# Optimization experiments

Hardware: AMD Instinct MI355X
Metric: run time of the kernel (lower is better)

The kernel has to match this reference:

```python
import jax, jax.numpy as jnp
import numpy as np
import math

WINDOW_LEFT = 512   # sliding-window: each query attends to keys in [q-512, q]
WINDOW_RIGHT = 0    # causal
NEG_INF = -1e30


def setup_inputs() -> dict:
    key = jax.random.key(0)
    kq, kk, kv, ks = jax.random.split(key, 4)
    B, S, H, D = 2, 2048, 16, 128
    q = jax.random.normal(kq, (B, S, H, D), dtype=jnp.float32)
    k = jax.random.normal(kk, (B, S, H, D), dtype=jnp.float32)
    v = jax.random.normal(kv, (B, S, H, D), dtype=jnp.float32)
    # geometric-ish ALiBi slopes per head (positive, decaying), like flash-attn
    alibi_slopes = jax.random.uniform(ks, (H,), dtype=jnp.float32, minval=0.001, maxval=0.5)
    return {"q": q, "k": k, "v": v, "alibi_slopes": alibi_slopes}


def reference(q, k, v, alibi_slopes):
    # q,k,v: [B, S, H, D]; alibi_slopes: [H]
    B, S, H, D = q.shape
    scale = 1.0 / math.sqrt(D)
    # scores: [B, H, Sq, Sk]
    scores = jnp.einsum("bqhd,bkhd->bhqk", q, k) * scale
    qi = jnp.arange(S)[:, None]
    ki = jnp.arange(S)[None, :]
    rel = ki - qi  # [Sq, Sk], <=0 for past keys
    # ALiBi bias (equal q/k lengths): -slope * |q - k|
    alibi = -alibi_slopes[:, None, None] * jnp.abs(rel).astype(scores.dtype)  # [H,Sq,Sk]
    scores = scores + alibi[None, :, :, :]
    # causal + sliding-window mask: allow WINDOW_RIGHT future, WINDOW_LEFT past
    mask = (rel <= WINDOW_RIGHT) & (rel >= -WINDOW_LEFT)  # [Sq, Sk]
    scores = jnp.where(mask[None, None, :, :], scores, NEG_INF)
    p = jax.nn.softmax(scores, axis=-1)
    out = jnp.einsum("bhqk,bkhd->bqhd", p, v)
    return out
```

## Files before the change

### kernel.cpp

```cpp
#include <hip/hip_runtime.h>
#include <hip/hip_bf16.h>

typedef __attribute__((ext_vector_type(8))) __bf16 bf16x8;
typedef __attribute__((ext_vector_type(4))) __bf16 bf16x4;
typedef __attribute__((ext_vector_type(2))) __bf16 bf16x2;
typedef __attribute__((ext_vector_type(4))) float f32x4;

#define MFMA32(a, b, c) __builtin_amdgcn_mfma_f32_16x16x32_bf16((a), (b), (c), 0, 0, 0)

constexpr int Bc = 2, Sc = 2048, Hc = 16, Dc = 128;
constexpr int HD = Hc * Dc;
constexpr int QB = 128;
constexpr float SCALE = 0.0883883476483184405f;
constexpr float NEGF = -30000.0f;
constexpr int KSTR = 2080;

__device__ inline bf16x8 cvt8(f32x4 a, f32x4 b) {
    bf16x8 r;
    r[0]=(__bf16)a[0]; r[1]=(__bf16)a[1]; r[2]=(__bf16)a[2]; r[3]=(__bf16)a[3];
    r[4]=(__bf16)b[0]; r[5]=(__bf16)b[1]; r[6]=(__bf16)b[2]; r[7]=(__bf16)b[3];
    return r;
}

__global__ __launch_bounds__(256, 2) void lumen_attn_kernel(
    const float* __restrict__ Q, const float* __restrict__ K,
    const float* __restrict__ V, const float* __restrict__ SLP,
    float* __restrict__ O)
{
    __shared__ __align__(16) char k_lds[64 * 256];
    __shared__ __align__(16) char v_lds[8 * KSTR];
    __shared__ __align__(16) char p_lds[4][32 * 128];

    const int tid  = threadIdx.x;
    const int lane = tid & 63;
    const int wid  = tid >> 6;
    const int cl = lane & 15;
    const int kg = lane >> 4;
    const int r0 = kg << 2;

    const int bid = blockIdx.x;
    const int swz = (bid & 7) * 64 + (bid >> 3);
    const int qb  = (swz & 15) * QB;
    const int bh  = swz >> 4;
    const int h = bh & 15, b = bh >> 4;

    const float slope = SLP[h];
    const size_t base = (size_t)b * Sc * HD + (size_t)h * Dc;
    const float* qp = Q + base;
    const float* kp = K + base;
    const float* vp = V + base;
    float*       op = O + base;

    const int qw = qb + wid * 32;

    bf16x8 qf[2][4];
    #pragma unroll
    for (int s = 0; s < 2; ++s) {
        const float* qrow = qp + (size_t)(qw + s * 16 + cl) * HD + kg * 8;
        #pragma unroll
        for (int c = 0; c < 4; ++c) {
            f32x4 a = *(const f32x4*)(qrow + c * 32);
            f32x4 bq = *(const f32x4*)(qrow + c * 32 + 4);
            #pragma unroll
            for (int i = 0; i < 4; ++i) { a[i] *= SCALE; bq[i] *= SCALE; }
            qf[s][c] = cvt8(a, bq);
        }
    }

    f32x4 o_acc[2][8];
    #pragma unroll
    for (int s = 0; s < 2; ++s)
        #pragma unroll
        for (int nn = 0; nn < 8; ++nn) o_acc[s][nn] = f32x4{0.f, 0.f, 0.f, 0.f};
    float ssum[2] = {0.f, 0.f};

    int voff[8];
    #pragma unroll
    for (int nn = 0; nn < 8; ++nn) {
        const int d = nn * 16 + cl;
        const int s = (d & ~7) | ((d & 7) ^ ((d >> 3) & 7));
        voff[nn] = s * 16;
    }

    const int kb0    = qb > 512 ? qb - 512 : 0;
    const int kb_end = qb + QB - 64;

    const int tk5 = tid >> 3;
    const int t8  = tid & 7;
    const int d0  = t8 * 16;

    char* const pw = p_lds[wid];
    const int swp = (cl & 7) << 4;

    for (int kb = kb0; kb <= kb_end; kb += 64) {
        __syncthreads();

        #pragma unroll
        for (int p = 0; p < 2; ++p) {
            const int k = p * 32 + tk5;
            const float* kr = kp + (size_t)(kb + k) * HD + d0;
            bf16x8 kA = cvt8(*(const f32x4*)kr,       *(const f32x4*)(kr + 4));
            bf16x8 kB = cvt8(*(const f32x4*)(kr + 8), *(const f32x4*)(kr + 12));
            char* kbse = k_lds + k * 256;
            const int sw = (k & 15) << 4;
            *(bf16x8*)(kbse + ((d0 * 2) ^ sw))      = kA;
            *(bf16x8*)(kbse + ((d0 * 2 + 16) ^ sw)) = kB;
        }
        {
            const float* v0_ = vp + (size_t)(kb + 2 * tk5) * HD + d0;
            const float* v1_ = v0_ + HD;
            bf16x8 vA0 = cvt8(*(const f32x4*)v0_,       *(const f32x4*)(v0_ + 4));
            bf16x8 vA1 = cvt8(*(const f32x4*)(v0_ + 8), *(const f32x4*)(v0_ + 12));
            bf16x8 vB0 = cvt8(*(const f32x4*)v1_,       *(const f32x4*)(v1_ + 4));
            bf16x8 vB1 = cvt8(*(const f32x4*)(v1_ + 8), *(const f32x4*)(v1_ + 12));
            char* vdst = v_lds + (tk5 >> 2) * KSTR + (tk5 & 3) * 4;
            #pragma unroll
            for (int j = 0; j < 8; ++j) {
                const int d = d0 + j;
                const int s = (d & ~7) | ((d & 7) ^ ((d >> 3) & 7));
                bf16x2 pk; pk[0] = vA0[j]; pk[1] = vB0[j];
                *(bf16x2*)(vdst + s * 16) = pk;
            }
            #pragma unroll
            for (int j = 0; j < 8; ++j) {
                const int d = d0 + 8 + j;
                const int s = (d & ~7) | ((d & 7) ^ ((d >> 3) & 7));
                bf16x2 pk; pk[0] = vA1[j]; pk[1] = vB1[j];
                *(bf16x2*)(vdst + s * 16) = pk;
            }
        }
        __syncthreads();

        if (kb > qw + 31 || kb + 63 < qw - 512) continue;

        #pragma unroll
        for (int n = 0; n < 4; ++n) {
            f32x4 s0 = f32x4{0.f, 0.f, 0.f, 0.f};
            f32x4 s1 = f32x4{0.f, 0.f, 0.f, 0.f};
            const char* kbse = k_lds + (n * 16 + cl) * 256;
            const int sw = cl << 4;
            #pragma unroll
            for (int c = 0; c < 4; ++c) {
                bf16x8 kf = *(const bf16x8*)(kbse + (((c * 32 + kg * 8) * 2) ^ sw));
                s0 = MFMA32(kf, qf[0][c], s0);
                s1 = MFMA32(kf, qf[1][c], s1);
            }
            const int poff = ((n * 16 + r0) * 2) ^ swp;
            #pragma unroll
            for (int s2 = 0; s2 < 2; ++s2) {
                const f32x4 sv = s2 ? s1 : s0;
                const int q = qw + s2 * 16 + cl;
                bf16x4 pk;
                #pragma unroll
                for (int j = 0; j < 4; ++j) {
                    const int rel = q - (kb + n * 16 + r0 + j);
                    const float val = ((unsigned)rel <= 512u)
                                      ? fmaf(-slope, (float)rel, sv[j]) : NEGF;
                    const float pe = __expf(val);
                    ssum[s2] += pe;
                    pk[j] = (__bf16)pe;
                }
                *(bf16x4*)(pw + (s2 * 16 + cl) * 128 + poff) = pk;
            }
        }

        asm volatile("s_waitcnt lgkmcnt(0)" ::: "memory");

        #pragma unroll
        for (int kk = 0; kk < 2; ++kk) {
            const int off = ((kk * 32 + kg * 8) * 2) ^ swp;
            bf16x8 pa0 = *(const bf16x8*)(pw + cl * 128 + off);
            bf16x8 pa1 = *(const bf16x8*)(pw + (16 + cl) * 128 + off);
            const char* vko = v_lds + (kk * 4 + kg) * KSTR;
            #pragma unroll
            for (int nn = 0; nn < 8; ++nn) {
                bf16x8 vf = *(const bf16x8*)(vko + voff[nn]);
                o_acc[0][nn] = MFMA32(pa0, vf, o_acc[0][nn]);
                o_acc[1][nn] = MFMA32(pa1, vf, o_acc[1][nn]);
            }
        }
    }

    #pragma unroll
    for (int s = 0; s < 2; ++s) {
        ssum[s] += __shfl_xor(ssum[s], 16);
        ssum[s] += __shfl_xor(ssum[s], 32);
    }
    #pragma unroll
    for (int s = 0; s < 2; ++s) {
        #pragma unroll
        for (int j = 0; j < 4; ++j) {
            const float sj = __shfl(ssum[s], r0 + j);
            const float inv = 1.0f / sj;
            float* orow = op + (size_t)(qw + s * 16 + r0 + j) * HD;
            #pragma unroll
            for (int nn = 0; nn < 8; ++nn)
                orow[nn * 16 + cl] = o_acc[s][nn][j] * inv;
        }
    }
}

extern "C" void kernel_launch(void* const* d_in, const int* in_sizes, int n_in,
                              void* d_out, int out_size, void* d_ws, size_t ws_size,
                              hipStream_t stream) {
    const float* q   = (const float*)d_in[0];
    const float* k   = (const float*)d_in[1];
    const float* v   = (const float*)d_in[2];
    const float* slp = (const float*)d_in[3];
    float* out = (float*)d_out;

    dim3 grid(Bc * Hc * (Sc / QB));
    lumen_attn_kernel<<<grid, dim3(256), 0, stream>>>(q, k, v, slp, out);
}
```

Before: 54.21 us.

## Double-buffer K/V tiles with register prefetch and enlarge query block to 256

Grows the query block from 128 to 256 rows with 8 waves per block, so each loaded K/V tile is shared by twice as many queries. It also double-buffers the K/V shared-memory tiles: the next tile's global loads are issued into registers before computing the current tile, then converted and written to the other buffer afterwards, leaving one barrier per iteration. This aims to hide global load latency and cut redundant K/V traffic. In exchange it uses more LDS and registers per block, and there are half as many blocks (256 for 256 CUs), which may reduce occupancy and load balance.

```diff
diff --git a/kernel.cpp b/kernel.cpp
--- a/kernel.cpp
+++ b/kernel.cpp
@@ -10,7 +10,7 @@
 
 constexpr int Bc = 2, Sc = 2048, Hc = 16, Dc = 128;
 constexpr int HD = Hc * Dc;
-constexpr int QB = 128;
+constexpr int QB = 256;
 constexpr float SCALE = 0.0883883476483184405f;
 constexpr float NEGF = -30000.0f;
 constexpr int KSTR = 2080;
@@ -22,14 +22,14 @@
     return r;
 }
 
-__global__ __launch_bounds__(256, 2) void lumen_attn_kernel(
+__global__ __launch_bounds__(512, 2) void lumen_attn_kernel(
     const float* __restrict__ Q, const float* __restrict__ K,
     const float* __restrict__ V, const float* __restrict__ SLP,
     float* __restrict__ O)
 {
-    __shared__ __align__(16) char k_lds[64 * 256];
-    __shared__ __align__(16) char v_lds[8 * KSTR];
-    __shared__ __align__(16) char p_lds[4][32 * 128];
+    __shared__ __align__(16) char k_lds[2][64 * 256];
+    __shared__ __align__(16) char v_lds[2][8 * KSTR];
+    __shared__ __align__(16) char p_lds[8][32 * 128];
 
     const int tid  = threadIdx.x;
     const int lane = tid & 63;
@@ -39,9 +39,9 @@
     const int r0 = kg << 2;
 
     const int bid = blockIdx.x;
-    const int swz = (bid & 7) * 64 + (bid >> 3);
-    const int qb  = (swz & 15) * QB;
-    const int bh  = swz >> 4;
+    const int swz = (bid & 7) * 32 + (bid >> 3);
+    const int qb  = (swz & 7) * QB;
+    const int bh  = swz >> 3;
     const int h = bh & 15, b = bh >> 4;
 
     const float slope = SLP[h];
@@ -84,100 +84,112 @@
 
     const int kb0    = qb > 512 ? qb - 512 : 0;
     const int kb_end = qb + QB - 64;
-
-    const int tk5 = tid >> 3;
-    const int t8  = tid & 7;
-    const int d0  = t8 * 16;
+    const int NT     = (kb_end - kb0) / 64 + 1;
+
+    const int ktk = tid >> 3;
+    const int kd0 = (tid & 7) * 16;
+    const int ksw = (ktk & 15) << 4;
+    const int vtk = tid >> 4;
+    const int vd0 = (tid & 15) * 8;
+    const int va_ = tid & 15;
 
     char* const pw = p_lds[wid];
     const int swp = (cl & 7) << 4;
 
-    for (int kb = kb0; kb <= kb_end; kb += 64) {
+    f32x4 ra, rb, rc, rd, sa, sb, sc, sd;
+
+    #define LOAD(kbn) do {                                                     \
+        const float* kr_ = kp + (size_t)((kbn) + ktk) * HD + kd0;              \
+        ra = *(const f32x4*)kr_;        rb = *(const f32x4*)(kr_ + 4);         \
+        rc = *(const f32x4*)(kr_ + 8);  rd = *(const f32x4*)(kr_ + 12);        \
+        const float* vr_ = vp + (size_t)((kbn) + 2 * vtk) * HD + vd0;          \
+        sa = *(const f32x4*)vr_;        sb = *(const f32x4*)(vr_ + 4);         \
+        sc = *(const f32x4*)(vr_ + HD); sd = *(const f32x4*)(vr_ + HD + 4);    \
+    } while (0)
+
+    #define WRITE(bi) do {                                                     \
+        bf16x8 kw0_ = cvt8(ra, rb), kw1_ = cvt8(rc, rd);                       \
+        char* kb_ = k_lds[bi] + ktk * 256;                                     \
+        *(bf16x8*)(kb_ + ((kd0 * 2) ^ ksw))      = kw0_;                       \
+        *(bf16x8*)(kb_ + ((kd0 * 2 + 16) ^ ksw)) = kw1_;                       \
+        bf16x8 vw0_ = cvt8(sa, sb), vw1_ = cvt8(sc, sd);                       \
+        char* vdst_ = v_lds[bi] + (vtk >> 2) * KSTR + (vtk & 3) * 4;           \
+        _Pragma("unroll")                                                      \
+        for (int j = 0; j < 8; ++j) {                                          \
+            const int s_ = va_ * 8 + (j ^ (va_ & 7));                          \
+            bf16x2 pk_; pk_[0] = vw0_[j]; pk_[1] = vw1_[j];                    \
+            *(bf16x2*)(vdst_ + s_ * 16) = pk_;                                 \
+        }                                                                      \
+    } while (0)
+
+    LOAD(kb0);
+    WRITE(0);
+
+    for (int i = 0; i < NT; ++i) {
+        const int kb  = kb0 + i * 64;
+        const int cur = i & 1;
         __syncthreads();
 
-        #pragma unroll
-        for (int p = 0; p < 2; ++p) {
-            const int k = p * 32 + tk5;
-            const float* kr = kp + (size_t)(kb + k) * HD + d0;
-            bf16x8 kA = cvt8(*(const f32x4*)kr,       *(const f32x4*)(kr + 4));
-            bf16x8 kB = cvt8(*(const f32x4*)(kr + 8), *(const f32x4*)(kr + 12));
-            char* kbse = k_lds + k * 256;
-            const int sw = (k & 15) << 4;
-            *(bf16x8*)(kbse + ((d0 * 2) ^ sw))      = kA;
-            *(bf16x8*)(kbse + ((d0 * 2 + 16) ^ sw)) = kB;
-        }
-        {
-            const float* v0_ = vp + (size_t)(kb + 2 * tk5) * HD + d0;
-            const float* v1_ = v0_ + HD;
-            bf16x8 vA0 = cvt8(*(const f32x4*)v0_,       *(const f32x4*)(v0_ + 4));
-            bf16x8 vA1 = cvt8(*(const f32x4*)(v0_ + 8), *(const f32x4*)(v0_ + 12));
-            bf16x8 vB0 = cvt8(*(const f32x4*)v1_,       *(const f32x4*)(v1_ + 4));
-            bf16x8 vB1 = cvt8(*(const f32x4*)(v1_ + 8), *(const f32x4*)(v1_ + 12));
-            char* vdst = v_lds + (tk5 >> 2) * KSTR + (tk5 & 3) * 4;
-            #pragma unroll
-            for (int j = 0; j < 8; ++j) {
-                const int d = d0 + j;
-                const int s = (d & ~7) | ((d & 7) ^ ((d >> 3) & 7));
-                bf16x2 pk; pk[0] = vA0[j]; pk[1] = vB0[j];
-                *(bf16x2*)(vdst + s * 16) = pk;
+        if (i + 1 < NT) {
+            LOAD(kb + 64);
+            __builtin_amdgcn_sched_barrier(0);
+        }
+
+        if (!(kb > qw + 31 || kb + 63 < qw - 512)) {
+            const char* kbuf = k_lds[cur];
+            const char* vbuf = v_lds[cur];
+
+            #pragma unroll
+            for (int n = 0; n < 4; ++n) {
+                f32x4 s0 = f32x4{0.f, 0.f, 0.f, 0.f};
+                f32x4 s1 = f32x4{0.f, 0.f, 0.f, 0.f};
+                const char* kbse = kbuf + (n * 16 + cl) * 256;
+                const int sw = cl << 4;
+                #pragma unroll
+                for (int c = 0; c < 4; ++c) {
+                    bf16x8 kf = *(const bf16x8*)(kbse + (((c * 32 + kg * 8) * 2) ^ sw));
+                    s0 = MFMA32(kf, qf[0][c], s0);
+                    s1 = MFMA32(kf, qf[1][c], s1);
+                }
+                const int poff = ((n * 16 + r0) * 2) ^ swp;
+                #pragma unroll
+                for (int s2 = 0; s2 < 2; ++s2) {
+                    const f32x4 sv = s2 ? s1 : s0;
+                    const int q = qw + s2 * 16 + cl;
+                    bf16x4 pk;
+                    #pragma unroll
+                    for (int j = 0; j < 4; ++j) {
+                        const int rel = q - (kb + n * 16 + r0 + j);
+                        const float val = ((unsigned)rel <= 512u)
+                                          ? fmaf(-slope, (float)rel, sv[j]) : NEGF;
+                        const float pe = __expf(val);
+                        ssum[s2] += pe;
+                        pk[j] = (__bf16)pe;
+                    }
+                    *(bf16x4*)(pw + (s2 * 16 + cl) * 128 + poff) = pk;
+                }
             }
-            #pragma unroll
-            for (int j = 0; j < 8; ++j) {
-                const int d = d0 + 8 + j;
-                const int s = (d & ~7) | ((d & 7) ^ ((d >> 3) & 7));
-                bf16x2 pk; pk[0] = vA1[j]; pk[1] = vB1[j];
-                *(bf16x2*)(vdst + s * 16) = pk;
+
+            asm volatile("s_waitcnt lgkmcnt(0)" ::: "memory");
+
+            #pragma unroll
+            for (int kk = 0; kk < 2; ++kk) {
+                const int off = ((kk * 32 + kg * 8) * 2) ^ swp;
+                bf16x8 pa0 = *(const bf16x8*)(pw + cl * 128 + off);
+                bf16x8 pa1 = *(const bf16x8*)(pw + (16 + cl) * 128 + off);
+                const char* vko = vbuf + (kk * 4 + kg) * KSTR;
+                #pragma unroll
+                for (int nn = 0; nn < 8; ++nn) {
+                    bf16x8 vf = *(const bf16x8*)(vko + voff[nn]);
+                    o_acc[0][nn] = MFMA32(pa0, vf, o_acc[0][nn]);
+                    o_acc[1][nn] = MFMA32(pa1, vf, o_acc[1][nn]);
+                }
             }
         }
-        __syncthreads();
-
-        if (kb > qw + 31 || kb + 63 < qw - 512) continue;
-
-        #pragma unroll
-        for (int n = 0; n < 4; ++n) {
-            f32x4 s0 = f32x4{0.f, 0.f, 0.f, 0.f};
-            f32x4 s1 = f32x4{0.f, 0.f, 0.f, 0.f};
-            const char* kbse = k_lds + (n * 16 + cl) * 256;
-            const int sw = cl << 4;
-            #pragma unroll
-            for (int c = 0; c < 4; ++c) {
-                bf16x8 kf = *(const bf16x8*)(kbse + (((c * 32 + kg * 8) * 2) ^ sw));
-                s0 = MFMA32(kf, qf[0][c], s0);
-                s1 = MFMA32(kf, qf[1][c], s1);
-            }
-            const int poff = ((n * 16 + r0) * 2) ^ swp;
-            #pragma unroll
-            for (int s2 = 0; s2 < 2; ++s2) {
-                const f32x4 sv = s2 ? s1 : s0;
-                const int q = qw + s2 * 16 + cl;
-                bf16x4 pk;
-                #pragma unroll
-                for (int j = 0; j < 4; ++j) {
-                    const int rel = q - (kb + n * 16 + r0 + j);
-                    const float val = ((unsigned)rel <= 512u)
-                                      ? fmaf(-slope, (float)rel, sv[j]) : NEGF;
-                    const float pe = __expf(val);
-                    ssum[s2] += pe;
-                    pk[j] = (__bf16)pe;
-                }
-                *(bf16x4*)(pw + (s2 * 16 + cl) * 128 + poff) = pk;
-            }
-        }
-
-        asm volatile("s_waitcnt lgkmcnt(0)" ::: "memory");
-
-        #pragma unroll
-        for (int kk = 0; kk < 2; ++kk) {
-            const int off = ((kk * 32 + kg * 8) * 2) ^ swp;
-            bf16x8 pa0 = *(const bf16x8*)(pw + cl * 128 + off);
-            bf16x8 pa1 = *(const bf16x8*)(pw + (16 + cl) * 128 + off);
-            const char* vko = v_lds + (kk * 4 + kg) * KSTR;
-            #pragma unroll
-            for (int nn = 0; nn < 8; ++nn) {
-                bf16x8 vf = *(const bf16x8*)(vko + voff[nn]);
-                o_acc[0][nn] = MFMA32(pa0, vf, o_acc[0][nn]);
-                o_acc[1][nn] = MFMA32(pa1, vf, o_acc[1][nn]);
-            }
+
+        if (i + 1 < NT) {
+            __builtin_amdgcn_sched_barrier(0);
+            WRITE(cur ^ 1);
         }
     }
 
@@ -198,6 +210,8 @@
                 orow[nn * 16 + cl] = o_acc[s][nn][j] * inv;
         }
     }
+    #undef LOAD
+    #undef WRITE
 }
 
 extern "C" void kernel_launch(void* const* d_in, const int* in_sizes, int n_in,
@@ -210,5 +224,5 @@
     float* out = (float*)d_out;
 
     dim3 grid(Bc * Hc * (Sc / QB));
-    lumen_attn_kernel<<<grid, dim3(256), 0, stream>>>(q, k, v, slp, out);
+    lumen_attn_kernel<<<grid, dim3(512), 0, stream>>>(q, k, v, slp, out);
 }
```

Result: faster. 47.89 us (-11.7%).
